# Kernel tuning notes

Hardware: AMD Instinct MI355X
Metric: run time of the kernel (lower is better)

Reference implementation:

```python
import jax, jax.numpy as jnp
import numpy as np

B, T, N, F = 16, 12, 1024, 8
H = 64        # hidden_size
K = 2         # diffusion order (DCRNN k == DiffConv gnn_kernel)
HORIZON = 12
E = 32 * N    # number of edges


def setup_inputs() -> dict:
    key = jax.random.key(0)
    ks = jax.random.split(key, 16)
    s = 0.05
    inp = {}
    inp['x'] = jax.random.normal(ks[0], (B, T, N, F), jnp.float32)
    inp['edge_index'] = jax.random.randint(ks[1], (2, E), 0, N)
    inp['edge_weight'] = jax.random.uniform(ks[2], (E,), jnp.float32)
    inp['adj'] = jax.random.uniform(ks[3], (N, N), jnp.float32)
    # encoder Linear(F -> H)
    inp['W_enc'] = jax.random.normal(ks[4], (F, H), jnp.float32) * s
    inp['b_enc'] = jnp.zeros((H,), jnp.float32)
    # NodeEmbedding(n_nodes, H)
    inp['node_emb'] = jax.random.normal(ks[5], (N, H), jnp.float32) * s
    # DCRNN gates: DenseGraphConvOrderK(2H -> H), 2 supports x K hops (include_self=False)
    gin = 2 * H * 2 * K
    inp['W_r'] = jax.random.normal(ks[6], (gin, H), jnp.float32) * s
    inp['b_r'] = jnp.zeros((H,), jnp.float32)
    inp['W_u'] = jax.random.normal(ks[7], (gin, H), jnp.float32) * s
    inp['b_u'] = jnp.zeros((H,), jnp.float32)
    inp['W_c'] = jax.random.normal(ks[8], (gin, H), jnp.float32) * s
    inp['b_c'] = jnp.zeros((H,), jnp.float32)
    # DiffConv filters: Linear(H*(2K+1) -> H), root_weight=True, add_backward=True
    din = H * (2 * K + 1)
    inp['W_diff'] = jax.random.normal(ks[9], (din, H), jnp.float32) * s
    inp['b_diff'] = jnp.zeros((H,), jnp.float32)
    # decoder Linear(H -> F*HORIZON)
    inp['W_dec'] = jax.random.normal(ks[10], (H, F * HORIZON), jnp.float32) * s
    inp['b_dec'] = jnp.zeros((F * HORIZON,), jnp.float32)
    return inp


def _dgconv(x, supports, W, b):
    # DenseGraphConvOrderK, include_self=False: for each support, K hop powers, concat on channels.
    feats = []
    for a in supports:  # a: [n, n], row-normalized transition matrix
        x1 = x
        for _ in range(K):
            x1 = jnp.einsum('bvc,wv->bwc', x1, a)
            feats.append(x1)
    return jnp.concatenate(feats, axis=-1) @ W + b


def _forward(x, edge_index, edge_weight, adj, W_enc, b_enc, node_emb,
             W_r, b_r, W_u, b_u, W_c, b_c, W_diff, b_diff, W_dec, b_dec):
    # --- DenseGraphConvOrderK.compute_support: fwd/bwd row-normalized transitions ---
    adj_fwd = adj / adj.sum(1, keepdims=True)
    adjT = adj.T
    adj_bwd = adjT / adjT.sum(1, keepdims=True)
    supports = (adj_fwd, adj_bwd)

    # encoder + node embeddings (broadcast over batch & time)
    x_enc = x @ W_enc + b_enc + node_emb  # [B, T, N, H]

    # --- DenseDCRNN: GRU with diffusion-conv gates, scan over time ---
    def step(h, xt):
        xh = jnp.concatenate([xt, h], axis=-1)                 # [B, N, 2H]
        r = jax.nn.sigmoid(_dgconv(xh, supports, W_r, b_r))    # forget/reset gate
        u = jax.nn.sigmoid(_dgconv(xh, supports, W_u, b_u))    # update gate
        xc = jnp.concatenate([xt, r * h], axis=-1)
        c = jnp.tanh(_dgconv(xc, supports, W_c, b_c))          # candidate
        h_new = u * h + (1.0 - u) * c
        return h_new, None

    h0 = jnp.zeros((B, N, H), x_enc.dtype)
    h, _ = jax.lax.scan(step, h0, jnp.swapaxes(x_enc, 0, 1))   # last state, [B, N, H]

    # --- DiffConv readout on sparse edge list (root + K fwd hops + K bwd hops) ---
    src, dst = edge_index[0], edge_index[1]

    def norm_w(group_idx):
        deg = jax.ops.segment_sum(edge_weight, group_idx, num_segments=N)
        inv = jnp.where(deg > 0, 1.0 / deg, 0.0)
        return edge_weight * inv[group_idx]

    w_fwd = norm_w(dst)  # normalize over target (dim=1)
    w_bwd = norm_w(src)  # flipped edges, normalized over their targets (= src)

    feats = [h]
    for s_, d_, w_ in ((src, dst, w_fwd), (dst, src, w_bwd)):
        xs = h
        for _ in range(K):
            msg = xs[:, s_, :] * w_[None, :, None]             # [B, E, H]
            xs = jnp.zeros_like(h).at[:, d_, :].add(msg)
            feats.append(xs)
    z = jnp.concatenate(feats, axis=-1) @ W_diff + b_diff      # [B, N, H]

    # decoder + rearrange 'b n (t f) -> b t n f'
    out = z @ W_dec + b_dec                                    # [B, N, HORIZON*F]
    return out.reshape(B, N, HORIZON, F).transpose(0, 2, 1, 3) # [B, HORIZON, N, F]


def reference(x, edge_index, edge_weight, adj, W_enc, b_enc, node_emb,
              W_r, b_r, W_u, b_u, W_c, b_c, W_diff, b_diff, W_dec, b_dec):
    return _forward(x, edge_index, edge_weight, adj, W_enc, b_enc, node_emb,
                    W_r, b_r, W_u, b_u, W_c, b_c, W_diff, b_diff, W_dec, b_dec)
```

## Files before the change

kernel.cpp:

```cpp
#include <hip/hip_runtime.h>
#include <math.h>

#define BB 16
#define TT 12
#define NN 1024
#define FF 8
#define HH 64
#define EE 32768
#define DIN 320
#define ODIM 96
#define APAD 40

typedef _Float16 v8h __attribute__((ext_vector_type(8)));
typedef float v4f __attribute__((ext_vector_type(4)));

__device__ __forceinline__ unsigned short f2h(float v) {
    _Float16 h = (_Float16)v;
    unsigned short u;
    __builtin_memcpy(&u, &h, 2);
    return u;
}
__device__ __forceinline__ float h2f(unsigned short u) {
    _Float16 h;
    __builtin_memcpy(&h, &u, 2);
    return (float)h;
}
__device__ __forceinline__ void gl_lds16(const void* g, void* l) {
    __builtin_amdgcn_global_load_lds(
        (const __attribute__((address_space(1))) unsigned int*)g,
        (__attribute__((address_space(3))) unsigned int*)l, 16, 0, 0);
}

__global__ void k_ei_detect(const int* __restrict__ ei_raw, int* __restrict__ flag) {
    __shared__ int s[256];
    s[threadIdx.x] = ei_raw[2 * threadIdx.x + 1];
    __syncthreads();
    for (int st = 128; st > 0; st >>= 1) {
        if (threadIdx.x < st) s[threadIdx.x] |= s[threadIdx.x + st];
        __syncthreads();
    }
    if (threadIdx.x == 0) flag[0] = (s[0] == 0) ? 1 : 0;
}
__global__ void k_ei_norm(const int* __restrict__ ei_raw, const int* __restrict__ flag,
                          int* __restrict__ ei32) {
    int j = blockIdx.x * 256 + threadIdx.x;
    ei32[j] = flag[0] ? ei_raw[2 * j] : ei_raw[j];
}

__global__ void k_rowsum(const float* __restrict__ adj, float* __restrict__ rinv) {
    __shared__ float s[256];
    int i = blockIdx.x;
    float acc = 0.f;
    for (int j = threadIdx.x; j < NN; j += 256) acc += adj[i * NN + j];
    s[threadIdx.x] = acc;
    __syncthreads();
    for (int st = 128; st > 0; st >>= 1) {
        if (threadIdx.x < st) s[threadIdx.x] += s[threadIdx.x + st];
        __syncthreads();
    }
    if (threadIdx.x == 0) rinv[i] = (s[0] != 0.f) ? 1.f / s[0] : 0.f;
}
__global__ void k_colsum(const float* __restrict__ adj, float* __restrict__ cinv) {
    int j = blockIdx.x * 256 + threadIdx.x;
    float acc = 0.f;
    for (int i = 0; i < NN; i++) acc += adj[i * NN + j];
    cinv[j] = (acc != 0.f) ? 1.f / acc : 0.f;
}

__global__ __launch_bounds__(256) void k_prepA(
        const float* __restrict__ adj, const float* __restrict__ rinv,
        const float* __restrict__ cinv, unsigned short* __restrict__ Mp) {
    int w0 = blockIdx.x * 64, v0 = blockIdx.y * 64;
    __shared__ float T[64][68];
    int row = threadIdx.x >> 2, cs = (threadIdx.x & 3) * 16;
    #pragma unroll
    for (int j = 0; j < 4; j++)
        *(float4*)&T[row][cs + j * 4] = *(const float4*)(adj + (size_t)(w0 + row) * NN + v0 + cs + j * 4);
    __syncthreads();
    {
        float sc = rinv[w0 + row];
        unsigned short h8[16];
        #pragma unroll
        for (int j = 0; j < 16; j++) h8[j] = f2h(T[row][cs + j] * sc);
        size_t ofs = (size_t)(w0 + row) * NN + v0 + cs;
        ((uint4*)(Mp + ofs))[0] = *(uint4*)&h8[0];
        ((uint4*)(Mp + ofs))[1] = *(uint4*)&h8[8];
    }
    {
        float sc = cinv[v0 + row];
        unsigned short h8[16];
        #pragma unroll
        for (int j = 0; j < 16; j++) h8[j] = f2h(T[cs + j][row] * sc);
        size_t ofs = (size_t)2048 * NN + (size_t)(v0 + row) * NN + w0 + cs;
        ((uint4*)(Mp + ofs))[0] = *(uint4*)&h8[0];
        ((uint4*)(Mp + ofs))[1] = *(uint4*)&h8[8];
    }
}

__global__ __launch_bounds__(256) void k_msq(unsigned short* __restrict__ M) {
    int zz = blockIdx.z;
    size_t srcb = (size_t)zz * 2048 * NN;
    size_t dstb = srcb + (size_t)1024 * NN;
    int w0 = blockIdx.x * 64, n0 = blockIdx.y * 64;

    __shared__ unsigned short sA[64 * APAD];
    __shared__ unsigned short sB[64 * APAD];

    int tid = threadIdx.x;
    int lane = tid & 63, wave = tid >> 6;
    int wr = (wave >> 1) * 32, wc = (wave & 1) * 32;
    int l15 = lane & 15, quad = lane >> 4;
    int arow = tid >> 2, akk = (tid & 3) * 8;
    int bkr = tid & 31, bc8 = (tid >> 5) * 8;

    v4f acc[2][2];
    #pragma unroll
    for (int i = 0; i < 2; i++)
        #pragma unroll
        for (int j = 0; j < 2; j++) { acc[i][j][0]=0.f; acc[i][j][1]=0.f; acc[i][j][2]=0.f; acc[i][j][3]=0.f; }

    for (int k0 = 0; k0 < NN; k0 += 32) {
        *(uint4*)&sA[arow * APAD + akk] = *(const uint4*)(M + srcb + (size_t)(w0 + arow) * NN + k0 + akk);
        uint4 bh = *(const uint4*)(M + srcb + (size_t)(k0 + bkr) * NN + n0 + bc8);
        const unsigned short* ph = (const unsigned short*)&bh;
        #pragma unroll
        for (int j = 0; j < 8; j++) sB[(bc8 + j) * APAD + bkr] = ph[j];
        __syncthreads();

        v8h a0 = *(const v8h*)&sA[(wr + l15) * APAD + quad * 8];
        v8h a1 = *(const v8h*)&sA[(wr + 16 + l15) * APAD + quad * 8];
        #pragma unroll
        for (int j = 0; j < 2; j++) {
            v8h bb = *(const v8h*)&sB[(wc + j * 16 + l15) * APAD + quad * 8];
            acc[0][j] = __builtin_amdgcn_mfma_f32_16x16x32_f16(a0, bb, acc[0][j], 0, 0, 0);
            acc[1][j] = __builtin_amdgcn_mfma_f32_16x16x32_f16(a1, bb, acc[1][j], 0, 0, 0);
        }
        __syncthreads();
    }

    #pragma unroll
    for (int i = 0; i < 2; i++)
        #pragma unroll
        for (int j = 0; j < 2; j++) {
            int rb = w0 + wr + i * 16 + quad * 4;
            int cc = n0 + wc + j * 16 + l15;
            #pragma unroll
            for (int rr = 0; rr < 4; rr++)
                M[dstb + (size_t)(rb + rr) * NN + cc] = f2h(acc[i][j][rr]);
        }
}

__global__ void k_m2frag(const unsigned short* __restrict__ P, unsigned short* __restrict__ F) {
    size_t t = (size_t)blockIdx.x * 256 + threadIdx.x;
    int rowloc = (int)(t & 63);
    int kc = (int)((t >> 6) & 127);
    int T = (int)(t >> 13);
    size_t src = ((size_t)(T * 64 + rowloc) * NN) + kc * 8;
    *(uint4*)(F + t * 8) = *(const uint4*)(P + src);
}

__global__ void k_xT(const float* __restrict__ x, unsigned short* __restrict__ XallT) {
    int bx = blockIdx.x;
    int t = bx >> 4, b = bx & 15;
    int tid = threadIdx.x;
    int f = tid & 7, half = tid >> 3;
    const float* xs = x + ((size_t)b * TT + t) * NN * FF + f;
    int n0 = half * 32;
    unsigned short v[32];
    #pragma unroll
    for (int i = 0; i < 32; i++) v[i] = f2h(xs[(size_t)(n0 + i) * FF]);
    unsigned short* dst = XallT + ((size_t)bx * 8 + f) * NN + n0;
    #pragma unroll
    for (int i = 0; i < 4; i++) *(uint4*)(dst + i * 8) = *(uint4*)&v[i * 8];
}
__global__ void k_embT(const float* __restrict__ emb, unsigned short* __restrict__ XallT) {
    int c = blockIdx.x;
    int n0 = threadIdx.x * 4;
    unsigned short v[4];
    #pragma unroll
    for (int j = 0; j < 4; j++) v[j] = f2h(emb[(size_t)(n0 + j) * HH + c]);
    *(uint2*)(XallT + (size_t)(1536 + c) * NN + n0) = *(uint2*)v;
}

__global__ __launch_bounds__(512) void k_hopX(
        const unsigned short* __restrict__ Mf,
        const unsigned short* __restrict__ XallT,
        unsigned short* __restrict__ AX, unsigned short* __restrict__ Eg) {
    int bid = blockIdx.x;
    int rt = bid & 31;
    int y  = bid >> 5;
    int g = rt >> 3;
    int n0 = (rt & 7) * 128;
    int c0 = y * 128;

    __shared__ unsigned short sA[2][16 * 512];
    __shared__ unsigned short sX[2][16 * 512];

    int tid = threadIdx.x;
    int lane = tid & 63, wave = tid >> 6;
    int rh = wave >> 2, cq = wave & 3;
    int l15 = lane & 15, quad = lane >> 4;

    v4f acc[4][2];
    #pragma unroll
    for (int i = 0; i < 4; i++)
        #pragma unroll
        for (int j = 0; j < 2; j++) { acc[i][j][0]=0.f; acc[i][j][1]=0.f; acc[i][j][2]=0.f; acc[i][j][3]=0.f; }

    auto STAGE = [&](int buf, int k0) {
        #pragma unroll
        for (int s = 0; s < 4; s++) {
            int id = wave + s * 8;
            if (id < 16) {
                int ah = id >> 3, kh = (id >> 2) & 1, rf = id & 3;
                const unsigned short* src = Mf +
                    ((size_t)(rt * 2 + ah) * 8192 +
                     (size_t)((k0 >> 3) + kh * 4 + quad) * 64 + rf * 16 + l15) * 8;
                gl_lds16(src, &sA[buf][id * 512]);
            } else {
                int xi = id - 16, cj = xi >> 1, kh = xi & 1;
                const unsigned short* src = XallT +
                    (size_t)(c0 + cj * 16 + l15) * NN + k0 + kh * 32 + quad * 8;
                gl_lds16(src, &sX[buf][xi * 512]);
            }
        }
    };

    STAGE(0, 0);
    STAGE(1, 64);

    int lu = lane * 8;
    for (int kt = 0; kt < 16; kt++) {
        int cur = kt & 1;
        if (kt < 15) asm volatile("s_waitcnt vmcnt(4)" ::: "memory");
        else         asm volatile("s_waitcnt vmcnt(0)" ::: "memory");
        __builtin_amdgcn_s_barrier();
        asm volatile("" ::: "memory");
        #pragma unroll
        for (int kh = 0; kh < 2; kh++) {
            v8h a[4], bx[2];
            #pragma unroll
            for (int rf = 0; rf < 4; rf++)
                a[rf] = *(const v8h*)&sA[cur][(rh * 8 + kh * 4 + rf) * 512 + lu];
            #pragma unroll
            for (int j = 0; j < 2; j++)
                bx[j] = *(const v8h*)&sX[cur][((cq * 2 + j) * 2 + kh) * 512 + lu];
            #pragma unroll
            for (int rf = 0; rf < 4; rf++)
                #pragma unroll
                for (int j = 0; j < 2; j++)
                    acc[rf][j] = __builtin_amdgcn_mfma_f32_16x16x32_f16(a[rf], bx[j], acc[rf][j], 0, 0, 0);
        }
        asm volatile("" ::: "memory");
        __builtin_amdgcn_s_barrier();
        asm volatile("" ::: "memory");
        if (kt < 14) STAGE(cur, (kt + 2) * 64);
    }

    #pragma unroll
    for (int rf = 0; rf < 4; rf++)
        #pragma unroll
        for (int j = 0; j < 2; j++) {
            int col = c0 + cq * 32 + j * 16 + l15;
            #pragma unroll
            for (int rr = 0; rr < 4; rr++) {
                int nrow = n0 + rh * 64 + rf * 16 + quad * 4 + rr;
                if (col < 1536) {
                    int tb = col >> 3, f = col & 7;
                    AX[((size_t)tb * NN + nrow) * 32 + g * 8 + f] = f2h(acc[rf][j][rr]);
                } else if (col < 1600) {
                    int cc = col - 1536;
                    Eg[((size_t)(g << 10) + nrow) * 64 + cc] = f2h(acc[rf][j][rr]);
                }
            }
        }
}

__global__ void k_veg(const float* __restrict__ W_enc,
                      const float* __restrict__ W_r, const float* __restrict__ W_u,
                      const float* __restrict__ W_c, float* __restrict__ Veg) {
    int idx = blockIdx.x * 256 + threadIdx.x;
    int c = idx & 63;
    int gf = (idx >> 6) & 31;
    int G = idx >> 11;
    int g = gf >> 3, f = gf & 7;
    const float* W = (G == 0) ? W_r : ((G == 1) ? W_u : W_c);
    float acc = 0.f;
    for (int c2 = 0; c2 < 64; c2++)
        acc += W_enc[f * HH + c2] * W[(size_t)(g * 128 + c2) * HH + c];
    Veg[idx] = acc;
}

__global__ void k_constE(const unsigned short* __restrict__ Eg, const float* __restrict__ b_enc,
                         const float* __restrict__ W_r, const float* __restrict__ W_u,
                         const float* __restrict__ W_c, float* __restrict__ constE) {
    int G = blockIdx.y;
    int n = blockIdx.x * 4 + (threadIdx.x >> 6);
    int c = threadIdx.x & 63;
    const float* W = (G == 0) ? W_r : ((G == 1) ? W_u : W_c);
    float acc = 0.f;
    for (int g = 0; g < 4; g++)
        for (int c2 = 0; c2 < 64; c2++)
            acc += (h2f(Eg[((size_t)(g << 10) + n) * 64 + c2]) + b_enc[c2]) *
                   W[(size_t)(g * 128 + c2) * HH + c];
    constE[((size_t)G << 16) + (size_t)n * 64 + c] = acc;
}

__global__ void k_wfragH(const float* __restrict__ W_r, const float* __restrict__ W_u,
                         const float* __restrict__ W_c,
                         unsigned short* __restrict__ Fr, unsigned short* __restrict__ Fu,
                         unsigned short* __restrict__ Fc) {
    int idx = blockIdx.x * 256 + threadIdx.x;
    int G = idx >> 14;
    int r = idx & 16383;
    int e = r & 7, l = (r >> 3) & 63;
    int rest = r >> 9;
    int ks = rest & 7, cj = rest >> 3;
    int c = cj * 16 + (l & 15);
    int k = ks * 32 + (l >> 4) * 8 + e;
    int g = k >> 6, c2 = k & 63;
    const float* W = (G == 0) ? W_r : ((G == 1) ? W_u : W_c);
    unsigned short* F = (G == 0) ? Fr : ((G == 1) ? Fu : Fc);
    F[r] = f2h(W[(size_t)(g * 128 + 64 + c2) * HH + c]);
}
__global__ void k_wfragX(const float* __restrict__ Veg, unsigned short* __restrict__ Wx) {
    int idx = blockIdx.x * 256 + threadIdx.x;
    int G = idx >> 11;
    int r = idx & 2047;
    int e = r & 7, l = (r >> 3) & 63;
    int cj = r >> 9;
    int c = cj * 16 + (l & 15);
    int k = (l >> 4) * 8 + e;
    Wx[idx] = f2h(Veg[(size_t)G * 2048 + (size_t)k * 64 + c]);
}

__global__ void k_wfragO(const float* __restrict__ W_diff, const float* __restrict__ W_dec,
                         unsigned short* __restrict__ Wf) {
    int idx = blockIdx.x * 256 + threadIdx.x;
    int e = idx & 7, l = (idx >> 3) & 63;
    int rest = idx >> 9;
    int ks = rest % 10, cj = rest / 10;
    int o = cj * 16 + (l & 15);
    int k = ks * 32 + (l >> 4) * 8 + e;
    float acc = 0.f;
    for (int c = 0; c < 64; c++) acc += W_diff[(size_t)k * HH + c] * W_dec[(size_t)c * ODIM + o];
    Wf[idx] = f2h(acc);
}
__global__ void k_bzd(const float* __restrict__ b_diff, const float* __restrict__ W_dec,
                      const float* __restrict__ b_dec, float* __restrict__ bzd) {
    int o = threadIdx.x;
    float acc = b_dec[o];
    for (int c = 0; c < 64; c++) acc += b_diff[c] * W_dec[(size_t)c * ODIM + o];
    bzd[o] = acc;
}

__global__ __launch_bounds__(512) void k_hopRU(
        const unsigned short* __restrict__ Mf,
        const unsigned short* __restrict__ XhH,
        const unsigned short* __restrict__ AXt,
        const unsigned short* __restrict__ WfrH, const unsigned short* __restrict__ WfuH,
        const unsigned short* __restrict__ Wxr, const unsigned short* __restrict__ Wxu,
        const float* __restrict__ b_r, const float* __restrict__ b_u,
        const float* __restrict__ constE,
        const float* __restrict__ h,
        unsigned short* __restrict__ XhR, float* __restrict__ ubuf) {
    int bid = blockIdx.x;
    int b = bid >> 4, nt = bid & 15;
    int n0 = nt * 64;

    __shared__ unsigned short S[2][40 * 512];

    int tid = threadIdx.x;
    int lane = tid & 63, wave = tid >> 6;
    int l15 = lane & 15, quad = lane >> 4;
    int g = wave >> 1, rh2 = wave & 1;

    const unsigned short* Xbase = XhH + (size_t)b * 64 * NN;

    v4f acc[2][4];
    #pragma unroll
    for (int i = 0; i < 2; i++)
        #pragma unroll
        for (int j = 0; j < 4; j++) { acc[i][j][0]=0.f; acc[i][j][1]=0.f; acc[i][j][2]=0.f; acc[i][j][3]=0.f; }

    auto STAGE = [&](int buf, int k0) {
        #pragma unroll
        for (int s = 0; s < 5; s++) {
            int id = wave + s * 8;
            if (id < 32) {
                int gg = id >> 3, kh = (id >> 2) & 1, rf = id & 3;
                const unsigned short* src = Mf +
                    ((size_t)(gg * 16 + nt) * 8192 +
                     (size_t)((k0 >> 3) + kh * 4 + quad) * 64 + rf * 16 + l15) * 8;
                gl_lds16(src, &S[buf][id * 512]);
            } else {
                int xi = id - 32, cj = xi >> 1, kh = xi & 1;
                const unsigned short* src = Xbase +
                    (size_t)(cj * 16 + l15) * NN + k0 + kh * 32 + quad * 8;
                gl_lds16(src, &S[buf][(32 + xi) * 512]);
            }
        }
    };

    STAGE(0, 0);
    STAGE(1, 64);

    int lu = lane * 8;
    for (int kt = 0; kt < 16; kt++) {
        int cur = kt & 1;
        if (kt < 15) asm volatile("s_waitcnt vmcnt(5)" ::: "memory");
        else         asm volatile("s_waitcnt vmcnt(0)" ::: "memory");
        __builtin_amdgcn_s_barrier();
        asm volatile("" ::: "memory");
        #pragma unroll
        for (int kh = 0; kh < 2; kh++) {
            v8h a[2], bx[4];
            #pragma unroll
            for (int i = 0; i < 2; i++)
                a[i] = *(const v8h*)&S[cur][(g * 8 + kh * 4 + rh2 * 2 + i) * 512 + lu];
            #pragma unroll
            for (int cj = 0; cj < 4; cj++)
                bx[cj] = *(const v8h*)&S[cur][(32 + cj * 2 + kh) * 512 + lu];
            #pragma unroll
            for (int i = 0; i < 2; i++)
                #pragma unroll
                for (int cj = 0; cj < 4; cj++)
                    acc[i][cj] = __builtin_amdgcn_mfma_f32_16x16x32_f16(a[i], bx[cj], acc[i][cj], 0, 0, 0);
        }
        asm volatile("" ::: "memory");
        __builtin_amdgcn_s_barrier();
        asm volatile("" ::: "memory");
        if (kt < 14) STAGE(cur, (kt + 2) * 64);
    }

    unsigned short* Yt = &S[0][0];
    #pragma unroll
    for (int i = 0; i < 2; i++)
        #pragma unroll
        for (int cj = 0; cj < 4; cj++) {
            int col = g * 64 + cj * 16 + l15;
            #pragma unroll
            for (int rr = 0; rr < 4; rr++) {
                int row = rh2 * 32 + i * 16 + quad * 4 + rr;
                Yt[row * 264 + col] = f2h(acc[i][cj][rr]);
            }
        }
    __syncthreads();

    int rw = wave & 3, gate = wave >> 2;
    const unsigned short* WH = gate ? WfuH : WfrH;
    const unsigned short* WX = gate ? Wxu : Wxr;
    const float* bias = gate ? b_u : b_r;
    const float* cE = constE + ((size_t)gate << 16);

    v4f acc2[4];
    #pragma unroll
    for (int cj = 0; cj < 4; cj++) { acc2[cj][0]=0.f; acc2[cj][1]=0.f; acc2[cj][2]=0.f; acc2[cj][3]=0.f; }

    {
        v8h ax = *(const v8h*)(AXt + ((size_t)(b << 10) + n0 + rw * 16 + l15) * 32 + quad * 8);
        #pragma unroll
        for (int cj = 0; cj < 4; cj++) {
            v8h bf = *(const v8h*)(WX + (size_t)cj * 512 + lu);
            acc2[cj] = __builtin_amdgcn_mfma_f32_16x16x32_f16(ax, bf, acc2[cj], 0, 0, 0);
        }
    }
    #pragma unroll
    for (int ks = 0; ks < 8; ks++) {
        v8h a = *(const v8h*)&Yt[(rw * 16 + l15) * 264 + ks * 32 + quad * 8];
        #pragma unroll
        for (int cj = 0; cj < 4; cj++) {
            v8h bf = *(const v8h*)(WH + (size_t)(cj * 8 + ks) * 512 + lu);
            acc2[cj] = __builtin_amdgcn_mfma_f32_16x16x32_f16(a, bf, acc2[cj], 0, 0, 0);
        }
    }

    unsigned short* sT = &S[1][0];
    if (gate == 0) {
        #pragma unroll
        for (int cj = 0; cj < 4; cj++) {
            int c = cj * 16 + l15;
            float bb = bias[c];
            #pragma unroll
            for (int rr = 0; rr < 4; rr++) {
                int nl = rw * 16 + quad * 4 + rr;
                size_t row = (size_t)(b << 10) + n0 + nl;
                float pre = acc2[cj][rr] + bb + cE[(size_t)(n0 + nl) * 64 + c];
                float r = 1.f / (1.f + expf(-pre));
                sT[c * 72 + nl] = f2h(r * h[row * 64 + c]);
            }
        }
    } else {
        #pragma unroll
        for (int cj = 0; cj < 4; cj++) {
            int c = cj * 16 + l15;
            float bb = bias[c];
            #pragma unroll
            for (int rr = 0; rr < 4; rr++) {
                int nl = rw * 16 + quad * 4 + rr;
                size_t row = (size_t)(b << 10) + n0 + nl;
                float pre = acc2[cj][rr] + bb + cE[(size_t)(n0 + nl) * 64 + c];
                ubuf[row * 64 + c] = 1.f / (1.f + expf(-pre));
            }
        }
    }
    __syncthreads();
    {
        int c = tid >> 3, n8 = (tid & 7) * 8;
        *(uint4*)(XhR + ((size_t)b * 64 + c) * NN + n0 + n8) = *(uint4*)&sT[c * 72 + n8];
    }
}

__global__ __launch_bounds__(512) void k_hopC(
        const unsigned short* __restrict__ Mf,
        const unsigned short* __restrict__ XhR,
        const unsigned short* __restrict__ AXt,
        const unsigned short* __restrict__ WfcH, const unsigned short* __restrict__ Wxc,
        const float* __restrict__ b_c,
        const float* __restrict__ constE,
        const float* __restrict__ ubuf,
        float* __restrict__ h, unsigned short* __restrict__ XhH) {
    int bid = blockIdx.x;
    int b = bid >> 4, nt = bid & 15;
    int n0 = nt * 64;

    __shared__ unsigned short S[2][40 * 512];

    int tid = threadIdx.x;
    int lane = tid & 63, wave = tid >> 6;
    int l15 = lane & 15, quad = lane >> 4;
    int g = wave >> 1, rh2 = wave & 1;

    const unsigned short* Xbase = XhR + (size_t)b * 64 * NN;

    v4f acc[2][4];
    #pragma unroll
    for (int i = 0; i < 2; i++)
        #pragma unroll
        for (int j = 0; j < 4; j++) { acc[i][j][0]=0.f; acc[i][j][1]=0.f; acc[i][j][2]=0.f; acc[i][j][3]=0.f; }

    auto STAGE = [&](int buf, int k0) {
        #pragma unroll
        for (int s = 0; s < 5; s++) {
            int id = wave + s * 8;
            if (id < 32) {
                int gg = id >> 3, kh = (id >> 2) & 1, rf = id & 3;
                const unsigned short* src = Mf +
                    ((size_t)(gg * 16 + nt) * 8192 +
                     (size_t)((k0 >> 3) + kh * 4 + quad) * 64 + rf * 16 + l15) * 8;
                gl_lds16(src, &S[buf][id * 512]);
            } else {
                int xi = id - 32, cj = xi >> 1, kh = xi & 1;
                const unsigned short* src = Xbase +
                    (size_t)(cj * 16 + l15) * NN + k0 + kh * 32 + quad * 8;
                gl_lds16(src, &S[buf][(32 + xi) * 512]);
            }
        }
    };

    STAGE(0, 0);
    STAGE(1, 64);

    int lu = lane * 8;
    for (int kt = 0; kt < 16; kt++) {
        int cur = kt & 1;
        if (kt < 15) asm volatile("s_waitcnt vmcnt(5)" ::: "memory");
        else         asm volatile("s_waitcnt vmcnt(0)" ::: "memory");
        __builtin_amdgcn_s_barrier();
        asm volatile("" ::: "memory");
        #pragma unroll
        for (int kh = 0; kh < 2; kh++) {
            v8h a[2], bx[4];
            #pragma unroll
            for (int i = 0; i < 2; i++)
                a[i] = *(const v8h*)&S[cur][(g * 8 + kh * 4 + rh2 * 2 + i) * 512 + lu];
            #pragma unroll
            for (int cj = 0; cj < 4; cj++)
                bx[cj] = *(const v8h*)&S[cur][(32 + cj * 2 + kh) * 512 + lu];
            #pragma unroll
            for (int i = 0; i < 2; i++)
                #pragma unroll
                for (int cj = 0; cj < 4; cj++)
                    acc[i][cj] = __builtin_amdgcn_mfma_f32_16x16x32_f16(a[i], bx[cj], acc[i][cj], 0, 0, 0);
        }
        asm volatile("" ::: "memory");
        __builtin_amdgcn_s_barrier();
        asm volatile("" ::: "memory");
        if (kt < 14) STAGE(cur, (kt + 2) * 64);
    }

    unsigned short* Yt = &S[0][0];
    #pragma unroll
    for (int i = 0; i < 2; i++)
        #pragma unroll
        for (int cj = 0; cj < 4; cj++) {
            int col = g * 64 + cj * 16 + l15;
            #pragma unroll
            for (int rr = 0; rr < 4; rr++) {
                int row = rh2 * 32 + i * 16 + quad * 4 + rr;
                Yt[row * 264 + col] = f2h(acc[i][cj][rr]);
            }
        }
    __syncthreads();

    int rw = wave & 3, ch = wave >> 2;
    const float* cE = constE + ((size_t)2 << 16);

    v4f acc2[2];
    #pragma unroll
    for (int j = 0; j < 2; j++) { acc2[j][0]=0.f; acc2[j][1]=0.f; acc2[j][2]=0.f; acc2[j][3]=0.f; }

    {
        v8h ax = *(const v8h*)(AXt + ((size_t)(b << 10) + n0 + rw * 16 + l15) * 32 + quad * 8);
        #pragma unroll
        for (int j = 0; j < 2; j++) {
            v8h bf = *(const v8h*)(Wxc + (size_t)(ch * 2 + j) * 512 + lu);
            acc2[j] = __builtin_amdgcn_mfma_f32_16x16x32_f16(ax, bf, acc2[j], 0, 0, 0);
        }
    }
    #pragma unroll
    for (int ks = 0; ks < 8; ks++) {
        v8h a = *(const v8h*)&Yt[(rw * 16 + l15) * 264 + ks * 32 + quad * 8];
        #pragma unroll
        for (int j = 0; j < 2; j++) {
            v8h bf = *(const v8h*)(WfcH + (size_t)((ch * 2 + j) * 8 + ks) * 512 + lu);
            acc2[j] = __builtin_amdgcn_mfma_f32_16x16x32_f16(a, bf, acc2[j], 0, 0, 0);
        }
    }

    unsigned short* sT = &S[1][0];
    #pragma unroll
    for (int j = 0; j < 2; j++) {
        int c = (ch * 2 + j) * 16 + l15;
        float bb = b_c[c];
        #pragma unroll
        for (int rr = 0; rr < 4; rr++) {
            int nl = rw * 16 + quad * 4 + rr;
            size_t row = (size_t)(b << 10) + n0 + nl;
            float pre = acc2[j][rr] + bb + cE[(size_t)(n0 + nl) * 64 + c];
            float cv = tanhf(pre);
            float u = ubuf[row * 64 + c];
            float hv = h[row * 64 + c];
            float hn = u * hv + (1.f - u) * cv;
            h[row * 64 + c] = hn;
            sT[c * 72 + nl] = f2h(hn);
        }
    }
    __syncthreads();
    {
        int c = tid >> 3, n8 = (tid & 7) * 8;
        *(uint4*)(XhH + ((size_t)b * 64 + c) * NN + n0 + n8) = *(uint4*)&sT[c * 72 + n8];
    }
}

__global__ __launch_bounds__(512) void k_hopA(
        const unsigned short* __restrict__ Mf,
        const unsigned short* __restrict__ Xb,
        unsigned short* __restrict__ Yout, int out_stride, int out_gmul, int out_off) {
    int bid = blockIdx.x;
    int rt = bid & 31;
    int bp = bid >> 5;
    int g = rt >> 3;
    int n0 = (rt & 7) * 128;

    __shared__ unsigned short sA[2][16 * 512];
    __shared__ unsigned short sX[2][16 * 512];

    int tid = threadIdx.x;
    int lane = tid & 63, wave = tid >> 6;
    int rh = wave >> 2, cq = wave & 3;
    int l15 = lane & 15, quad = lane >> 4;

    const unsigned short* Xbase = Xb + (size_t)(bp * 2) * 64 * NN;

    v4f acc[4][2];
    #pragma unroll
    for (int i = 0; i < 4; i++)
        #pragma unroll
        for (int j = 0; j < 2; j++) { acc[i][j][0]=0.f; acc[i][j][1]=0.f; acc[i][j][2]=0.f; acc[i][j][3]=0.f; }

    auto STAGE = [&](int buf, int k0) {
        #pragma unroll
        for (int s = 0; s < 4; s++) {
            int id = wave + s * 8;
            if (id < 16) {
                int ah = id >> 3, kh = (id >> 2) & 1, rf = id & 3;
                const unsigned short* src = Mf +
                    ((size_t)(rt * 2 + ah) * 8192 +
                     (size_t)((k0 >> 3) + kh * 4 + quad) * 64 + rf * 16 + l15) * 8;
                gl_lds16(src, &sA[buf][id * 512]);
            } else {
                int xi = id - 16, cj = xi >> 1, kh = xi & 1;
                const unsigned short* src = Xbase +
                    (size_t)(cj * 16 + l15) * NN + k0 + kh * 32 + quad * 8;
                gl_lds16(src, &sX[buf][xi * 512]);
            }
        }
    };

    STAGE(0, 0);
    STAGE(1, 64);

    int lu = lane * 8;
    for (int kt = 0; kt < 16; kt++) {
        int cur = kt & 1;
        if (kt < 15) asm volatile("s_waitcnt vmcnt(4)" ::: "memory");
        else         asm volatile("s_waitcnt vmcnt(0)" ::: "memory");
        __builtin_amdgcn_s_barrier();
        asm volatile("" ::: "memory");
        #pragma unroll
        for (int kh = 0; kh < 2; kh++) {
            v8h a[4], bx[2];
            #pragma unroll
            for (int rf = 0; rf < 4; rf++)
                a[rf] = *(const v8h*)&sA[cur][(rh * 8 + kh * 4 + rf) * 512 + lu];
            #pragma unroll
            for (int j = 0; j < 2; j++)
                bx[j] = *(const v8h*)&sX[cur][((cq * 2 + j) * 2 + kh) * 512 + lu];
            #pragma unroll
            for (int rf = 0; rf < 4; rf++)
                #pragma unroll
                for (int j = 0; j < 2; j++)
                    acc[rf][j] = __builtin_amdgcn_mfma_f32_16x16x32_f16(a[rf], bx[j], acc[rf][j], 0, 0, 0);
        }
        asm volatile("" ::: "memory");
        __builtin_amdgcn_s_barrier();
        asm volatile("" ::: "memory");
        if (kt < 14) STAGE(cur, (kt + 2) * 64);
    }

    #pragma unroll
    for (int rf = 0; rf < 4; rf++)
        #pragma unroll
        for (int j = 0; j < 2; j++) {
            int colloc = cq * 32 + j * 16 + l15;
            int b = bp * 2 + (colloc >> 6);
            int c = colloc & 63;
            unsigned short* Y = Yout + (size_t)b * NN * out_stride + out_gmul * g + out_off + c;
            int rbase = n0 + rh * 64 + rf * 16 + quad * 4;
            #pragma unroll
            for (int rr = 0; rr < 4; rr++)
                Y[(size_t)(rbase + rr) * out_stride] = f2h(acc[rf][j][rr]);
        }
}

__global__ __launch_bounds__(256) void k_out(
        const unsigned short* __restrict__ featd,
        const unsigned short* __restrict__ Wf_o, const float* __restrict__ bzd,
        float* __restrict__ out) {
    int row0 = blockIdx.x * 64;
    int tid = threadIdx.x, lane = tid & 63, wave = tid >> 6;
    int l15 = lane & 15, quad = lane >> 4;

    v4f acc[6];
    #pragma unroll
    for (int cj = 0; cj < 6; cj++) { acc[cj][0]=0.f; acc[cj][1]=0.f; acc[cj][2]=0.f; acc[cj][3]=0.f; }

    const unsigned short* fbase = featd + (size_t)(row0 + wave * 16 + l15) * DIN + quad * 8;
    #pragma unroll 2
    for (int ks = 0; ks < 10; ks++) {
        v8h a = *(const v8h*)(fbase + ks * 32);
        #pragma unroll
        for (int cj = 0; cj < 6; cj++) {
            v8h bf = *(const v8h*)(Wf_o + (size_t)(cj * 10 + ks) * 512 + lane * 8);
            acc[cj] = __builtin_amdgcn_mfma_f32_16x16x32_f16(a, bf, acc[cj], 0, 0, 0);
        }
    }
    #pragma unroll
    for (int cj = 0; cj < 6; cj++) {
        int o = cj * 16 + l15;
        int t = o >> 3, f = o & 7;
        float bb = bzd[o];
        #pragma unroll
        for (int rr = 0; rr < 4; rr++) {
            int row = row0 + wave * 16 + quad * 4 + rr;
            int b = row >> 10, n = row & 1023;
            out[(((size_t)b * TT + t) * NN + n) * FF + f] = acc[cj][rr] + bb;
        }
    }
}

__global__ void k_deg(const int* __restrict__ ei32, const float* __restrict__ ew,
                      float* __restrict__ degd, float* __restrict__ degs) {
    int e = blockIdx.x * 256 + threadIdx.x;
    float w = ew[e];
    atomicAdd(&degd[ei32[EE + e]], w);
    atomicAdd(&degs[ei32[e]], w);
}
__global__ void k_spadd(const int* __restrict__ ei32, const float* __restrict__ ew,
                        const float* __restrict__ degd, const float* __restrict__ degs,
                        float* __restrict__ temp) {
    int e = blockIdx.x * 256 + threadIdx.x;
    int s = ei32[e], d = ei32[EE + e];
    float w = ew[e];
    float dd = degd[d], ds = degs[s];
    float wfv = dd > 0.f ? w / dd : 0.f;
    float wbv = ds > 0.f ? w / ds : 0.f;
    atomicAdd(&temp[(size_t)d * NN + s], wfv);
    atomicAdd(&temp[(size_t)NN * NN + (size_t)s * NN + d], wbv);
}
__global__ void k_spconv(const float* __restrict__ temp, unsigned short* __restrict__ Mp) {
    size_t i0 = ((size_t)blockIdx.x * 256 + threadIdx.x) * 8;
    size_t dst = (i0 < (size_t)NN * NN) ? i0 : i0 + (size_t)NN * NN;
    unsigned short h8[8];
    #pragma unroll
    for (int j = 0; j < 8; j++) h8[j] = f2h(temp[i0 + j]);
    *(uint4*)(Mp + dst) = *(uint4*)h8;
}

__global__ void k_featd_h(const float* __restrict__ h, unsigned short* __restrict__ featd) {
    size_t idx = (size_t)blockIdx.x * 256 + threadIdx.x;
    size_t row = idx >> 6; int c = (int)(idx & 63);
    featd[row * DIN + c] = f2h(h[idx]);
}

extern "C" void kernel_launch(void* const* d_in, const int* in_sizes, int n_in,
                              void* d_out, int out_size, void* d_ws, size_t ws_size,
                              hipStream_t stream) {
    const float* x      = (const float*)d_in[0];
    const int*   eiraw  = (const int*)  d_in[1];
    const float* ew     = (const float*)d_in[2];
    const float* adj    = (const float*)d_in[3];
    const float* W_enc  = (const float*)d_in[4];
    const float* b_enc  = (const float*)d_in[5];
    const float* emb    = (const float*)d_in[6];
    const float* W_r    = (const float*)d_in[7];
    const float* b_r    = (const float*)d_in[8];
    const float* W_u    = (const float*)d_in[9];
    const float* b_u    = (const float*)d_in[10];
    const float* W_c    = (const float*)d_in[11];
    const float* b_c    = (const float*)d_in[12];
    const float* W_diff = (const float*)d_in[13];
    const float* b_diff = (const float*)d_in[14];
    const float* W_dec  = (const float*)d_in[15];
    const float* b_dec  = (const float*)d_in[16];

    unsigned short* Mf    = (unsigned short*)d_ws;
    unsigned short* XhH   = Mf + (size_t)4096 * NN;
    unsigned short* XhR   = XhH + (size_t)BB * 64 * NN;
    unsigned short* featd = XhR + (size_t)BB * 64 * NN;
    float* h    = (float*)(featd + (size_t)BB * NN * DIN);
    float* ubuf = h + (size_t)BB * NN * HH;
    unsigned short* AXall = (unsigned short*)(ubuf + (size_t)BB * NN * HH);
    unsigned short* Mp    = AXall;
    unsigned short* XallT = AXall + (size_t)192 * NN * 32;
    unsigned short* Eg    = XallT + (size_t)1600 * NN;
    float* sptmp  = (float*)(Eg + (size_t)4 * NN * 64);
    float* constE = sptmp + (size_t)2 * NN * NN;
    float* Veg    = constE + (size_t)3 * NN * 64;
    unsigned short* WfH  = (unsigned short*)(Veg + 3 * 32 * 64);
    unsigned short* WfrH = WfH;
    unsigned short* WfuH = WfH + 16384;
    unsigned short* WfcH = WfH + 32768;
    unsigned short* Wx   = WfH + 49152;
    unsigned short* Wf_o = Wx + 6144;
    float* bzd  = (float*)(Wf_o + 30720);
    float* rinv = bzd + ODIM;
    float* cinv = rinv + NN;
    int*   eifl = (int*)(cinv + NN);
    int*   ei32 = eifl + 4;
    float* degd = (float*)(ei32 + 2 * EE);
    float* degs = degd + NN;

    hipMemsetAsync(h, 0, (size_t)BB * NN * HH * 4, stream);
    hipMemsetAsync(XhH, 0, (size_t)BB * 64 * NN * 2, stream);

    k_rowsum<<<NN, 256, 0, stream>>>(adj, rinv);
    k_colsum<<<NN / 256, 256, 0, stream>>>(adj, cinv);
    k_prepA<<<dim3(16, 16), 256, 0, stream>>>(adj, rinv, cinv, Mp);
    k_msq<<<dim3(16, 16, 2), 256, 0, stream>>>(Mp);
    k_m2frag<<<2048, 256, 0, stream>>>(Mp, Mf);

    k_xT<<<TT * BB, 256, 0, stream>>>(x, XallT);
    k_embT<<<64, 256, 0, stream>>>(emb, XallT);
    k_hopX<<<13 * 32, 512, 0, stream>>>(Mf, XallT, AXall, Eg);
    k_veg<<<24, 256, 0, stream>>>(W_enc, W_r, W_u, W_c, Veg);
    k_constE<<<dim3(256, 3), 256, 0, stream>>>(Eg, b_enc, W_r, W_u, W_c, constE);
    k_wfragH<<<192, 256, 0, stream>>>(W_r, W_u, W_c, WfrH, WfuH, WfcH);
    k_wfragX<<<24, 256, 0, stream>>>(Veg, Wx);
    k_wfragO<<<120, 256, 0, stream>>>(W_diff, W_dec, Wf_o);
    k_bzd<<<1, ODIM, 0, stream>>>(b_diff, W_dec, b_dec, bzd);

    for (int t = 0; t < TT; t++) {
        const unsigned short* AXt = AXall + (size_t)t * BB * NN * 32;
        k_hopRU<<<256, 512, 0, stream>>>(Mf, XhH, AXt, WfrH, WfuH, Wx, Wx + 2048,
                                         b_r, b_u, constE, h, XhR, ubuf);
        k_hopC<<<256, 512, 0, stream>>>(Mf, XhR, AXt, WfcH, Wx + 4096,
                                        b_c, constE, ubuf, h, XhH);
    }

    k_ei_detect<<<1, 256, 0, stream>>>(eiraw, eifl);
    k_ei_norm<<<2 * EE / 256, 256, 0, stream>>>(eiraw, eifl, ei32);
    hipMemsetAsync(degd, 0, (size_t)2 * NN * 4, stream);
    hipMemsetAsync(sptmp, 0, (size_t)2 * NN * NN * 4, stream);
    k_deg<<<EE / 256, 256, 0, stream>>>(ei32, ew, degd, degs);
    k_spadd<<<EE / 256, 256, 0, stream>>>(ei32, ew, degd, degs, sptmp);
    k_spconv<<<2 * NN * NN / (256 * 8), 256, 0, stream>>>(sptmp, Mp);
    k_msq<<<dim3(16, 16, 2), 256, 0, stream>>>(Mp);
    k_m2frag<<<2048, 256, 0, stream>>>(Mp, Mf);
    k_featd_h<<<BB * NN * HH / 256, 256, 0, stream>>>(h, featd);
    k_hopA<<<8 * 32, 512, 0, stream>>>(Mf, XhH, featd, DIN, 64, 64);
    k_out<<<BB * NN / 64, 256, 0, stream>>>(featd, Wf_o, bzd, (float*)d_out);
}
```

Measured before the change: 722.5 us.

## Halve node tile in recurrent hop kernels and parallelize column sums

The per-timestep hopRU/hopC kernels now work on 32-node tiles instead of 64, doubling the grid from 256 to 512 blocks so more of the GPU's compute units are busy during the 24 sequential launches. Shared staging, MFMA tiling, gate epilogues and output writes are remapped to match. The serial column-sum kernel is replaced by a parallel partial-sum kernel using atomics, followed by a separate reciprocal kernel. The cost is that each X tile is reloaded twice as often from memory, each block does less MFMA work per staged byte, and setup gains an extra memset and kernel launch.

```diff
diff --git a/kernel.cpp b/kernel.cpp
--- a/kernel.cpp
+++ b/kernel.cpp
@@ -60,11 +60,25 @@
     }
     if (threadIdx.x == 0) rinv[i] = (s[0] != 0.f) ? 1.f / s[0] : 0.f;
 }
-__global__ void k_colsum(const float* __restrict__ adj, float* __restrict__ cinv) {
+__global__ void k_colsumP(const float* __restrict__ adj, float* __restrict__ csum) {
+    int bi = blockIdx.x;
+    int j4 = threadIdx.x * 4;
+    float4 acc = {0.f, 0.f, 0.f, 0.f};
+    const float* base = adj + (size_t)bi * 16 * NN + j4;
+    #pragma unroll
+    for (int r = 0; r < 16; r++) {
+        float4 v = *(const float4*)(base + (size_t)r * NN);
+        acc.x += v.x; acc.y += v.y; acc.z += v.z; acc.w += v.w;
+    }
+    atomicAdd(&csum[j4 + 0], acc.x);
+    atomicAdd(&csum[j4 + 1], acc.y);
+    atomicAdd(&csum[j4 + 2], acc.z);
+    atomicAdd(&csum[j4 + 3], acc.w);
+}
+__global__ void k_cinv(const float* __restrict__ csum, float* __restrict__ cinv) {
     int j = blockIdx.x * 256 + threadIdx.x;
-    float acc = 0.f;
-    for (int i = 0; i < NN; i++) acc += adj[i * NN + j];
-    cinv[j] = (acc != 0.f) ? 1.f / acc : 0.f;
+    float s = csum[j];
+    cinv[j] = (s != 0.f) ? 1.f / s : 0.f;
 }
 
 __global__ __launch_bounds__(256) void k_prepA(
@@ -365,39 +379,39 @@
         const float* __restrict__ h,
         unsigned short* __restrict__ XhR, float* __restrict__ ubuf) {
     int bid = blockIdx.x;
-    int b = bid >> 4, nt = bid & 15;
-    int n0 = nt * 64;
-
-    __shared__ unsigned short S[2][40 * 512];
+    int b = bid >> 5, nth = bid & 31;
+    int nt = nth >> 1, hb = nth & 1;
+    int n0 = nth * 32;
+
+    __shared__ unsigned short S[2][24 * 512];
 
     int tid = threadIdx.x;
     int lane = tid & 63, wave = tid >> 6;
     int l15 = lane & 15, quad = lane >> 4;
-    int g = wave >> 1, rh2 = wave & 1;
+    int g = wave >> 1, rh = wave & 1;
 
     const unsigned short* Xbase = XhH + (size_t)b * 64 * NN;
 
-    v4f acc[2][4];
-    #pragma unroll
-    for (int i = 0; i < 2; i++)
-        #pragma unroll
-        for (int j = 0; j < 4; j++) { acc[i][j][0]=0.f; acc[i][j][1]=0.f; acc[i][j][2]=0.f; acc[i][j][3]=0.f; }
+    v4f acc[4];
+    #pragma unroll
+    for (int j = 0; j < 4; j++) { acc[j][0]=0.f; acc[j][1]=0.f; acc[j][2]=0.f; acc[j][3]=0.f; }
 
     auto STAGE = [&](int buf, int k0) {
         #pragma unroll
-        for (int s = 0; s < 5; s++) {
+        for (int s = 0; s < 3; s++) {
             int id = wave + s * 8;
-            if (id < 32) {
-                int gg = id >> 3, kh = (id >> 2) & 1, rf = id & 3;
+            if (id < 16) {
+                int gg = id >> 2, kh = (id >> 1) & 1, rfi = id & 1;
+                int rf = hb * 2 + rfi;
                 const unsigned short* src = Mf +
                     ((size_t)(gg * 16 + nt) * 8192 +
                      (size_t)((k0 >> 3) + kh * 4 + quad) * 64 + rf * 16 + l15) * 8;
                 gl_lds16(src, &S[buf][id * 512]);
             } else {
-                int xi = id - 32, cj = xi >> 1, kh = xi & 1;
+                int xi = id - 16, cj = xi >> 1, kh = xi & 1;
                 const unsigned short* src = Xbase +
                     (size_t)(cj * 16 + l15) * NN + k0 + kh * 32 + quad * 8;
-                gl_lds16(src, &S[buf][(32 + xi) * 512]);
+                gl_lds16(src, &S[buf][id * 512]);
             }
         }
     };
@@ -408,24 +422,18 @@
     int lu = lane * 8;
     for (int kt = 0; kt < 16; kt++) {
         int cur = kt & 1;
-        if (kt < 15) asm volatile("s_waitcnt vmcnt(5)" ::: "memory");
+        if (kt < 15) asm volatile("s_waitcnt vmcnt(3)" ::: "memory");
         else         asm volatile("s_waitcnt vmcnt(0)" ::: "memory");
         __builtin_amdgcn_s_barrier();
         asm volatile("" ::: "memory");
         #pragma unroll
         for (int kh = 0; kh < 2; kh++) {
-            v8h a[2], bx[4];
-            #pragma unroll
-            for (int i = 0; i < 2; i++)
-                a[i] = *(const v8h*)&S[cur][(g * 8 + kh * 4 + rh2 * 2 + i) * 512 + lu];
-            #pragma unroll
-            for (int cj = 0; cj < 4; cj++)
-                bx[cj] = *(const v8h*)&S[cur][(32 + cj * 2 + kh) * 512 + lu];
-            #pragma unroll
-            for (int i = 0; i < 2; i++)
-                #pragma unroll
-                for (int cj = 0; cj < 4; cj++)
-                    acc[i][cj] = __builtin_amdgcn_mfma_f32_16x16x32_f16(a[i], bx[cj], acc[i][cj], 0, 0, 0);
+            v8h a = *(const v8h*)&S[cur][(g * 4 + kh * 2 + rh) * 512 + lu];
+            #pragma unroll
+            for (int cj = 0; cj < 4; cj++) {
+                v8h bx = *(const v8h*)&S[cur][(16 + cj * 2 + kh) * 512 + lu];
+                acc[cj] = __builtin_amdgcn_mfma_f32_16x16x32_f16(a, bx, acc[cj], 0, 0, 0);
+            }
         }
         asm volatile("" ::: "memory");
         __builtin_amdgcn_s_barrier();
@@ -435,79 +443,77 @@
 
     unsigned short* Yt = &S[0][0];
     #pragma unroll
-    for (int i = 0; i < 2; i++)
-        #pragma unroll
-        for (int cj = 0; cj < 4; cj++) {
-            int col = g * 64 + cj * 16 + l15;
-            #pragma unroll
-            for (int rr = 0; rr < 4; rr++) {
-                int row = rh2 * 32 + i * 16 + quad * 4 + rr;
-                Yt[row * 264 + col] = f2h(acc[i][cj][rr]);
-            }
-        }
+    for (int cj = 0; cj < 4; cj++) {
+        int col = g * 64 + cj * 16 + l15;
+        #pragma unroll
+        for (int rr = 0; rr < 4; rr++) {
+            int row = rh * 16 + quad * 4 + rr;
+            Yt[row * 264 + col] = f2h(acc[cj][rr]);
+        }
+    }
     __syncthreads();
 
-    int rw = wave & 3, gate = wave >> 2;
+    int gate = wave >> 2, rw = (wave >> 1) & 1, ch = wave & 1;
     const unsigned short* WH = gate ? WfuH : WfrH;
     const unsigned short* WX = gate ? Wxu : Wxr;
     const float* bias = gate ? b_u : b_r;
     const float* cE = constE + ((size_t)gate << 16);
 
-    v4f acc2[4];
-    #pragma unroll
-    for (int cj = 0; cj < 4; cj++) { acc2[cj][0]=0.f; acc2[cj][1]=0.f; acc2[cj][2]=0.f; acc2[cj][3]=0.f; }
+    v4f acc2[2];
+    #pragma unroll
+    for (int j = 0; j < 2; j++) { acc2[j][0]=0.f; acc2[j][1]=0.f; acc2[j][2]=0.f; acc2[j][3]=0.f; }
 
     {
         v8h ax = *(const v8h*)(AXt + ((size_t)(b << 10) + n0 + rw * 16 + l15) * 32 + quad * 8);
         #pragma unroll
-        for (int cj = 0; cj < 4; cj++) {
-            v8h bf = *(const v8h*)(WX + (size_t)cj * 512 + lu);
-            acc2[cj] = __builtin_amdgcn_mfma_f32_16x16x32_f16(ax, bf, acc2[cj], 0, 0, 0);
+        for (int j = 0; j < 2; j++) {
+            v8h bf = *(const v8h*)(WX + (size_t)(ch * 2 + j) * 512 + lu);
+            acc2[j] = __builtin_amdgcn_mfma_f32_16x16x32_f16(ax, bf, acc2[j], 0, 0, 0);
         }
     }
     #pragma unroll
     for (int ks = 0; ks < 8; ks++) {
         v8h a = *(const v8h*)&Yt[(rw * 16 + l15) * 264 + ks * 32 + quad * 8];
         #pragma unroll
-        for (int cj = 0; cj < 4; cj++) {
-            v8h bf = *(const v8h*)(WH + (size_t)(cj * 8 + ks) * 512 + lu);
-            acc2[cj] = __builtin_amdgcn_mfma_f32_16x16x32_f16(a, bf, acc2[cj], 0, 0, 0);
+        for (int j = 0; j < 2; j++) {
+            v8h bf = *(const v8h*)(WH + (size_t)((ch * 2 + j) * 8 + ks) * 512 + lu);
+            acc2[j] = __builtin_amdgcn_mfma_f32_16x16x32_f16(a, bf, acc2[j], 0, 0, 0);
         }
     }
 
     unsigned short* sT = &S[1][0];
     if (gate == 0) {
         #pragma unroll
-        for (int cj = 0; cj < 4; cj++) {
-            int c = cj * 16 + l15;
+        for (int j = 0; j < 2; j++) {
+            int c = (ch * 2 + j) * 16 + l15;
             float bb = bias[c];
             #pragma unroll
             for (int rr = 0; rr < 4; rr++) {
                 int nl = rw * 16 + quad * 4 + rr;
                 size_t row = (size_t)(b << 10) + n0 + nl;
-                float pre = acc2[cj][rr] + bb + cE[(size_t)(n0 + nl) * 64 + c];
+                float pre = acc2[j][rr] + bb + cE[(size_t)(n0 + nl) * 64 + c];
                 float r = 1.f / (1.f + expf(-pre));
-                sT[c * 72 + nl] = f2h(r * h[row * 64 + c]);
+                sT[c * 36 + nl] = f2h(r * h[row * 64 + c]);
             }
         }
     } else {
         #pragma unroll
-        for (int cj = 0; cj < 4; cj++) {
-            int c = cj * 16 + l15;
+        for (int j = 0; j < 2; j++) {
+            int c = (ch * 2 + j) * 16 + l15;
             float bb = bias[c];
             #pragma unroll
             for (int rr = 0; rr < 4; rr++) {
                 int nl = rw * 16 + quad * 4 + rr;
                 size_t row = (size_t)(b << 10) + n0 + nl;
-                float pre = acc2[cj][rr] + bb + cE[(size_t)(n0 + nl) * 64 + c];
+                float pre = acc2[j][rr] + bb + cE[(size_t)(n0 + nl) * 64 + c];
                 ubuf[row * 64 + c] = 1.f / (1.f + expf(-pre));
             }
         }
     }
     __syncthreads();
     {
-        int c = tid >> 3, n8 = (tid & 7) * 8;
-        *(uint4*)(XhR + ((size_t)b * 64 + c) * NN + n0 + n8) = *(uint4*)&sT[c * 72 + n8];
+        int c = tid >> 3, n4 = (tid & 7) * 4;
+        *(uint2*)(XhR + ((size_t)b * 64 + c) * NN + n0 + n4) = *(uint2*)&sT[c * 36 + n4];
     }
 }
 
@@ -521,39 +527,39 @@
         const float* __restrict__ ubuf,
         float* __restrict__ h, unsigned short* __restrict__ XhH) {
     int bid = blockIdx.x;
-    int b = bid >> 4, nt = bid & 15;
-    int n0 = nt * 64;
-
-    __shared__ unsigned short S[2][40 * 512];
+    int b = bid >> 5, nth = bid & 31;
+    int nt = nth >> 1, hb = nth & 1;
+    int n0 = nth * 32;
+
+    __shared__ unsigned short S[2][24 * 512];
 
     int tid = threadIdx.x;
     int lane = tid & 63, wave = tid >> 6;
     int l15 = lane & 15, quad = lane >> 4;
-    int g = wave >> 1, rh2 = wave & 1;
+    int g = wave >> 1, rh = wave & 1;
 
     const unsigned short* Xbase = XhR + (size_t)b * 64 * NN;
 
-    v4f acc[2][4];
-    #pragma unroll
-    for (int i = 0; i < 2; i++)
-        #pragma unroll
-        for (int j = 0; j < 4; j++) { acc[i][j][0]=0.f; acc[i][j][1]=0.f; acc[i][j][2]=0.f; acc[i][j][3]=0.f; }
+    v4f acc[4];
+    #pragma unroll
+    for (int j = 0; j < 4; j++) { acc[j][0]=0.f; acc[j][1]=0.f; acc[j][2]=0.f; acc[j][3]=0.f; }
 
     auto STAGE = [&](int buf, int k0) {
         #pragma unroll
-        for (int s = 0; s < 5; s++) {
+        for (int s = 0; s < 3; s++) {
             int id = wave + s * 8;
-            if (id < 32) {
-                int gg = id >> 3, kh = (id >> 2) & 1, rf = id & 3;
+            if (id < 16) {
+                int gg = id >> 2, kh = (id >> 1) & 1, rfi = id & 1;
+                int rf = hb * 2 + rfi;
                 const unsigned short* src = Mf +
                     ((size_t)(gg * 16 + nt) * 8192 +
                      (size_t)((k0 >> 3) + kh * 4 + quad) * 64 + rf * 16 + l15) * 8;
                 gl_lds16(src, &S[buf][id * 512]);
             } else {
-                int xi = id - 32, cj = xi >> 1, kh = xi & 1;
+                int xi = id - 16, cj = xi >> 1, kh = xi & 1;
                 const unsigned short* src = Xbase +
                     (size_t)(cj * 16 + l15) * NN + k0 + kh * 32 + quad * 8;
-                gl_lds16(src, &S[buf][(32 + xi) * 512]);
+                gl_lds16(src, &S[buf][id * 512]);
             }
         }
     };
@@ -564,24 +570,18 @@
     int lu = lane * 8;
     for (int kt = 0; kt < 16; kt++) {
         int cur = kt & 1;
-        if (kt < 15) asm volatile("s_waitcnt vmcnt(5)" ::: "memory");
+        if (kt < 15) asm volatile("s_waitcnt vmcnt(3)" ::: "memory");
         else         asm volatile("s_waitcnt vmcnt(0)" ::: "memory");
         __builtin_amdgcn_s_barrier();
         asm volatile("" ::: "memory");
         #pragma unroll
         for (int kh = 0; kh < 2; kh++) {
-            v8h a[2], bx[4];
-            #pragma unroll
-            for (int i = 0; i < 2; i++)
-                a[i] = *(const v8h*)&S[cur][(g * 8 + kh * 4 + rh2 * 2 + i) * 512 + lu];
-            #pragma unroll
-            for (int cj = 0; cj < 4; cj++)
-                bx[cj] = *(const v8h*)&S[cur][(32 + cj * 2 + kh) * 512 + lu];
-            #pragma unroll
-            for (int i = 0; i < 2; i++)
-                #pragma unroll
-                for (int cj = 0; cj < 4; cj++)
-                    acc[i][cj] = __builtin_amdgcn_mfma_f32_16x16x32_f16(a[i], bx[cj], acc[i][cj], 0, 0, 0);
+            v8h a = *(const v8h*)&S[cur][(g * 4 + kh * 2 + rh) * 512 + lu];
+            #pragma unroll
+            for (int cj = 0; cj < 4; cj++) {
+                v8h bx = *(const v8h*)&S[cur][(16 + cj * 2 + kh) * 512 + lu];
+                acc[cj] = __builtin_amdgcn_mfma_f32_16x16x32_f16(a, bx, acc[cj], 0, 0, 0);
+            }
         }
         asm volatile("" ::: "memory");
         __builtin_amdgcn_s_barrier();
@@ -591,65 +591,55 @@
 
     unsigned short* Yt = &S[0][0];
     #pragma unroll
-    for (int i = 0; i < 2; i++)
-        #pragma unroll
-        for (int cj = 0; cj < 4; cj++) {
-            int col = g * 64 + cj * 16 + l15;
-            #pragma unroll
-            for (int rr = 0; rr < 4; rr++) {
-                int row = rh2 * 32 + i * 16 + quad * 4 + rr;
-                Yt[row * 264 + col] = f2h(acc[i][cj][rr]);
-            }
-        }
+    for (int cj = 0; cj < 4; cj++) {
+        int col = g * 64 + cj * 16 + l15;
+        #pragma unroll
+        for (int rr = 0; rr < 4; rr++) {
+            int row = rh * 16 + quad * 4 + rr;
+            Yt[row * 264 + col] = f2h(acc[cj][rr]);
+        }
+    }
     __syncthreads();
 
-    int rw = wave & 3, ch = wave >> 2;
+    int ch = wave >> 1, rw = wave & 1;
     const float* cE = constE + ((size_t)2 << 16);
 
-    v4f acc2[2];
-    #pragma unroll
-    for (int j = 0; j < 2; j++) { acc2[j][0]=0.f; acc2[j][1]=0.f; acc2[j][2]=0.f; acc2[j][3]=0.f; }
+    v4f acc2;
+    acc2[0]=0.f; acc2[1]=0.f; acc2[2]=0.f; acc2[3]=0.f;
 
     {
         v8h ax = *(const v8h*)(AXt + ((size_t)(b << 10) + n0 + rw * 16 + l15) * 32 + quad * 8);
-        #pragma unroll
-        for (int j = 0; j < 2; j++) {
-            v8h bf = *(const v8h*)(Wxc + (size_t)(ch * 2 + j) * 512 + lu);
-            acc2[j] = __builtin_amdgcn_mfma_f32_16x16x32_f16(ax, bf, acc2[j], 0, 0, 0);
-        }
+        v8h bf = *(const v8h*)(Wxc + (size_t)ch * 512 + lu);
+        acc2 = __builtin_amdgcn_mfma_f32_16x16x32_f16(ax, bf, acc2, 0, 0, 0);
     }
     #pragma unroll
     for (int ks = 0; ks < 8; ks++) {
         v8h a = *(const v8h*)&Yt[(rw * 16 + l15) * 264 + ks * 32 + quad * 8];
-        #pragma unroll
-        for (int j = 0; j < 2; j++) {
-            v8h bf = *(const v8h*)(WfcH + (size_t)((ch * 2 + j) * 8 + ks) * 512 + lu);
-            acc2[j] = __builtin_amdgcn_mfma_f32_16x16x32_f16(a, bf, acc2[j], 0, 0, 0);
-        }
+        v8h bf = *(const v8h*)(WfcH + (size_t)(ch * 8 + ks) * 512 + lu);
+        acc2 = __builtin_amdgcn_mfma_f32_16x16x32_f16(a, bf, acc2, 0, 0, 0);
     }
 
     unsigned short* sT = &S[1][0];
-    #pragma unroll
-    for (int j = 0; j < 2; j++) {
-        int c = (ch * 2 + j) * 16 + l15;
+    {
+        int c = ch * 16 + l15;
         float bb = b_c[c];
         #pragma unroll
         for (int rr = 0; rr < 4; rr++) {
             int nl = rw * 16 + quad * 4 + rr;
             size_t row = (size_t)(b << 10) + n0 + nl;
-            float pre = acc2[j][rr] + bb + cE[(size_t)(n0 + nl) * 64 + c];
+            float pre = acc2[rr] + bb + cE[(size_t)(n0 + nl) * 64 + c];
             float cv = tanhf(pre);
             float u = ubuf[row * 64 + c];
             float hv = h[row * 64 + c];
             float hn = u * hv + (1.f - u) * cv;
             h[row * 64 + c] = hn;
-            sT[c * 72 + nl] = f2h(hn);
+            sT[c * 36 + nl] = f2h(hn);
         }
     }
     __syncthreads();
     {
-        int c = tid >> 3, n8 = (tid & 7) * 8;
-        *(uint4*)(XhH + ((size_t)b * 64 + c) * NN + n0 + n8) = *(uint4*)&sT[c * 72 + n8];
+        int c = tid >> 3, n4 = (tid & 7) * 4;
+        *(uint2*)(XhH + ((size_t)b * 64 + c) * NN + n0 + n4) = *(uint2*)&sT[c * 36 + n4];
     }
 }
 
@@ -861,12 +851,15 @@
     int*   ei32 = eifl + 4;
     float* degd = (float*)(ei32 + 2 * EE);
     float* degs = degd + NN;
+    float* csum = degs + NN;
 
     hipMemsetAsync(h, 0, (size_t)BB * NN * HH * 4, stream);
     hipMemsetAsync(XhH, 0, (size_t)BB * 64 * NN * 2, stream);
+    hipMemsetAsync(csum, 0, NN * 4, stream);
 
     k_rowsum<<<NN, 256, 0, stream>>>(adj, rinv);
-    k_colsum<<<NN / 256, 256, 0, stream>>>(adj, cinv);
+    k_colsumP<<<64, 256, 0, stream>>>(adj, csum);
+    k_cinv<<<NN / 256, 256, 0, stream>>>(csum, cinv);
     k_prepA<<<dim3(16, 16), 256, 0, stream>>>(adj, rinv, cinv, Mp);
     k_msq<<<dim3(16, 16, 2), 256, 0, stream>>>(Mp);
     k_m2frag<<<2048, 256, 0, stream>>>(Mp, Mf);
@@ -883,9 +876,9 @@
 
     for (int t = 0; t < TT; t++) {
         const unsigned short* AXt = AXall + (size_t)t * BB * NN * 32;
-        k_hopRU<<<256, 512, 0, stream>>>(Mf, XhH, AXt, WfrH, WfuH, Wx, Wx + 2048,
+        k_hopRU<<<512, 512, 0, stream>>>(Mf, XhH, AXt, WfrH, WfuH, Wx, Wx + 2048,
                                          b_r, b_u, constE, h, XhR, ubuf);
-        k_hopC<<<256, 512, 0, stream>>>(Mf, XhR, AXt, WfcH, Wx + 4096,
+        k_hopC<<<512, 512, 0, stream>>>(Mf, XhR, AXt, WfcH, Wx + 4096,
                                         b_c, constE, ubuf, h, XhH);
     }
 
```

Result: no change. 722.1 us (-0.1%).
